# Kernel optimization log

Hardware: AMD Instinct MI355X
Metric: run time of the kernel (lower is better)

The kernel has to match this reference:

```python
import jax, jax.numpy as jnp
import numpy as np

N, C, K = 65536, 128, 16

def setup_inputs() -> dict:
    key = jax.random.key(0)
    ks = jax.random.split(key, 16)
    def w(k, i, o):
        return jax.random.normal(k, (i, o), dtype=jnp.float32) / np.sqrt(i)
    inp = {
        "x": jax.random.normal(ks[0], (N, C), dtype=jnp.float32),
        "coords": jax.random.normal(ks[1], (N, 3), dtype=jnp.float32) * 10.0,
        "neighbor_idx": jax.random.randint(ks[2], (N, K), 0, N, dtype=jnp.int32),
        # linear_top / linear_down (1x1 Minkowski convs, BN folded into affine)
        "W_top": w(ks[3], C, C), "b_top": jnp.zeros((C,), jnp.float32),
        "W_down": w(ks[4], C, C), "b_down": jnp.zeros((C,), jnp.float32),
        # phi (query), psi (key), alpha (value) 1x1 convs
        "W_phi": w(ks[5], C, C), "b_phi": jnp.zeros((C,), jnp.float32),
        "W_psi": w(ks[6], C, C), "b_psi": jnp.zeros((C,), jnp.float32),
        "W_alpha": w(ks[7], C, C), "b_alpha": jnp.zeros((C,), jnp.float32),
        # delta: positional-encoding MLP on relative xyz (3 -> C -> C)
        "W_d1": w(ks[8], 3, C), "b_d1": jnp.zeros((C,), jnp.float32),
        "W_d2": w(ks[9], C, C), "b_d2": jnp.zeros((C,), jnp.float32),
        # gamma: attention MLP (C -> C -> C), vector attention
        "W_g1": w(ks[10], C, C), "b_g1": jnp.zeros((C,), jnp.float32),
        "W_g2": w(ks[11], C, C), "b_g2": jnp.zeros((C,), jnp.float32),
    }
    return inp

def reference(x, coords, W_top, b_top, W_down, b_down, W_phi, b_phi, W_psi, b_psi,
              W_alpha, b_alpha, W_d1, b_d1, W_d2, b_d2, W_g1, b_g1, W_g2, b_g2,
              neighbor_idx):
    # linear_top
    h = x @ W_top + b_top                                  # (N, C)
    phi = h @ W_phi + b_phi                                # (N, C) query
    psi = h @ W_psi + b_psi                                # (N, C) key
    alpha = h @ W_alpha + b_alpha                          # (N, C) value
    # gather neighbor features / coords (irregular access)
    nb_psi = psi[neighbor_idx]                             # (N, K, C)
    nb_alpha = alpha[neighbor_idx]                         # (N, K, C)
    rel = coords[:, None, :] - coords[neighbor_idx]        # (N, K, 3)
    # delta: relative positional encoding MLP
    pos = jax.nn.relu(rel @ W_d1 + b_d1) @ W_d2 + b_d2     # (N, K, C)
    # vector attention: gamma(phi_i - psi_j + delta)
    attn_in = phi[:, None, :] - nb_psi + pos               # (N, K, C)
    logits = jax.nn.relu(attn_in @ W_g1 + b_g1) @ W_g2 + b_g2
    w = jax.nn.softmax(logits, axis=1)                     # softmax over K neighbors
    y = jnp.sum(w * (nb_alpha + pos), axis=1)              # (N, C)
    # linear_down + residual
    return y @ W_down + b_down + x
```

## Files before the change

kernel.cpp:

```cpp
#include <hip/hip_runtime.h>
#include <math.h>

#define C 128
#define K 16
#define M 4
#define ROWS 64

typedef unsigned short ushort_t;
typedef unsigned int u32;
typedef float f32x4 __attribute__((ext_vector_type(4)));
typedef _Float16 f16x8 __attribute__((ext_vector_type(8)));

union U8h { _Float16 h[8]; uint4 u; };

__device__ __forceinline__ float f16tof(ushort_t b) {
    _Float16 h = __builtin_bit_cast(_Float16, b); return (float)h;
}
__device__ __forceinline__ ushort_t ftof16(float f) {
    _Float16 h = (_Float16)f; return __builtin_bit_cast(ushort_t, h);
}
__device__ __forceinline__ f32x4 mfma16(f16x8 a, f16x8 b, f32x4 c) {
    return __builtin_amdgcn_mfma_f32_16x16x32_f16(a, b, c, 0, 0, 0);
}

__global__ __launch_bounds__(128) void k_prep(
    const float* __restrict__ s0, const float* __restrict__ s1,
    const float* __restrict__ s2, const float* __restrict__ s3,
    ushort_t* __restrict__ d0, ushort_t* __restrict__ d1,
    ushort_t* __restrict__ d2, ushort_t* __restrict__ d3)
{
    const int m = blockIdx.x >> 7, n = blockIdx.x & 127, e = threadIdx.x;
    const float* s = (m==0) ? s0 : (m==1) ? s1 : (m==2) ? s2 : s3;
    ushort_t*   d = (m==0) ? d0 : (m==1) ? d1 : (m==2) ? d2 : d3;
    d[n*C + e] = ftof16(s[e*C + n]);
}

__global__ __launch_bounds__(512) void k_qkv2(
    const float* __restrict__ x,
    const ushort_t* __restrict__ WTt, const float* __restrict__ bt,
    const ushort_t* __restrict__ WTp, const float* __restrict__ bp,
    const ushort_t* __restrict__ WTs, const float* __restrict__ bs,
    const ushort_t* __restrict__ WTa, const float* __restrict__ ba,
    ushort_t* __restrict__ phiB, ushort_t* __restrict__ psiB,
    ushort_t* __restrict__ alfB)
{
    __shared__ ushort_t sX[64*C];
    __shared__ ushort_t sH[64*C];
    const int tid = threadIdx.x, lane = tid & 63, wv = tid >> 6;
    const int ncol = (wv<<4) + (lane&15), arow = lane&15;
    const int kgrp = lane>>4, krow0 = kgrp<<3;
    const int r0 = blockIdx.x * 64;

    {
        const int rX = tid>>3, cX = (tid&7)<<4;
        const float* xp = &x[(size_t)(r0+rX)*C + cX];
        #pragma unroll
        for (int hf = 0; hf < 2; ++hf) {
            const float4 a  = *(const float4*)&xp[hf*8 + 0];
            const float4 b2 = *(const float4*)&xp[hf*8 + 4];
            U8h v;
            v.h[0]=(_Float16)a.x;  v.h[1]=(_Float16)a.y;
            v.h[2]=(_Float16)a.z;  v.h[3]=(_Float16)a.w;
            v.h[4]=(_Float16)b2.x; v.h[5]=(_Float16)b2.y;
            v.h[6]=(_Float16)b2.z; v.h[7]=(_Float16)b2.w;
            const int col = cX + hf*8;
            *(uint4*)&sX[(rX<<7) + (col ^ ((rX&7)<<3))] = v.u;
        }
    }
    __syncthreads();

    {
        f16x8 bf[4]; f32x4 hacc[4];
        #pragma unroll
        for (int kk = 0; kk < 4; ++kk)
            bf[kk] = *(const f16x8*)&WTt[(size_t)ncol*C + (kk<<5) + krow0];
        #pragma unroll
        for (int m = 0; m < 4; ++m) hacc[m] = (f32x4){0.f,0.f,0.f,0.f};
        __builtin_amdgcn_s_setprio(1);
        #pragma unroll
        for (int m = 0; m < 4; ++m)
            #pragma unroll
            for (int kk = 0; kk < 4; ++kk) {
                const int row = (m<<4) + arow;
                const f16x8 af = *(const f16x8*)&sX[(row<<7) + (((kk<<5)+krow0) ^ ((arow&7)<<3))];
                hacc[m] = mfma16(af, bf[kk], hacc[m]);
            }
        __builtin_amdgcn_s_setprio(0);
        const float btc = bt[ncol];
        #pragma unroll
        for (int m = 0; m < 4; ++m)
            #pragma unroll
            for (int r = 0; r < 4; ++r) {
                const int row = (m<<4) + (kgrp<<2) + r;
                sH[(row<<7) + (ncol ^ ((row&7)<<3))] = ftof16(hacc[m][r] + btc);
            }
    }
    __syncthreads();

#define OGEMM(WT_, b_, o_)                                                    \
    {                                                                         \
        f16x8 wf[4]; f32x4 oacc[4];                                           \
        _Pragma("unroll")                                                     \
        for (int kk = 0; kk < 4; ++kk)                                        \
            wf[kk] = *(const f16x8*)&WT_[(size_t)ncol*C + (kk<<5) + krow0];   \
        _Pragma("unroll")                                                     \
        for (int m = 0; m < 4; ++m) oacc[m] = (f32x4){0.f,0.f,0.f,0.f};      \
        __builtin_amdgcn_s_setprio(1);                                        \
        _Pragma("unroll")                                                     \
        for (int m = 0; m < 4; ++m)                                           \
            _Pragma("unroll")                                                 \
            for (int kk = 0; kk < 4; ++kk) {                                  \
                const int row = (m<<4) + arow;                                \
                const f16x8 af = *(const f16x8*)&sH[(row<<7) + (((kk<<5)+krow0) ^ ((arow&7)<<3))]; \
                oacc[m] = mfma16(af, wf[kk], oacc[m]);                        \
            }                                                                 \
        __builtin_amdgcn_s_setprio(0);                                        \
        const float bc = b_[ncol];                                            \
        _Pragma("unroll")                                                     \
        for (int m = 0; m < 4; ++m)                                           \
            _Pragma("unroll")                                                 \
            for (int r = 0; r < 4; ++r) {                                     \
                const int row = (m<<4) + (kgrp<<2) + r;                       \
                o_[(size_t)(r0+row)*C + ncol] = ftof16(oacc[m][r] + bc);      \
            }                                                                 \
    }
    OGEMM(WTp, bp, phiB)
    OGEMM(WTs, bs, psiB)
    OGEMM(WTa, ba, alfB)
#undef OGEMM
}

__global__ __launch_bounds__(512, 4) void k_attn7(
    const ushort_t* __restrict__ phiB, const ushort_t* __restrict__ psiB,
    const ushort_t* __restrict__ alfB,
    const float* __restrict__ coords, const int* __restrict__ nidx,
    const float* __restrict__ Wd1, const float* __restrict__ bd1,
    const ushort_t* __restrict__ WTd2, const float* __restrict__ bd2,
    const ushort_t* __restrict__ WTg1, const float* __restrict__ bg1,
    const ushort_t* __restrict__ WTg2,
    ushort_t* __restrict__ yB,
    int ngroups, int gpb)
{
    __shared__ ushort_t sT0[ROWS*C];
    __shared__ ushort_t sT1[ROWS*C];
    __shared__ ushort_t sA[ROWS*C];
    __shared__ float    sWd1[3][C];
    __shared__ float    sbd1v[C];

    const int tid  = threadIdx.x, lane = tid & 63, wv = tid >> 6;
    const int ncol = (wv<<4) + (lane&15);
    const int arow = lane & 15;
    const int kgrp = lane >> 4, krow0 = kgrp << 3;
    const int grow = tid >> 3;
    const int gpt  = grow >> 4;
    const int gk   = grow & 15;
    const int gc   = (tid & 7) << 4;

    const int g0 = blockIdx.x * gpb;
    if (g0 >= ngroups) return;
    const int gend = (g0 + gpb < ngroups) ? (g0 + gpb) : ngroups;

    if (tid < 3*C) ((float*)sWd1)[tid] = Wd1[tid];
    else if (tid < 4*C) sbd1v[tid - 3*C] = bd1[tid - 3*C];

    f16x8 wd2[4];
    #pragma unroll
    for (int kk = 0; kk < 4; ++kk)
        wd2[kk] = *(const f16x8*)&WTd2[(size_t)ncol*C + (kk<<5) + krow0];
    const float bd2c = bd2[ncol], bg1c = bg1[ncol];

    __syncthreads();

    int jP; float cn0,cn1,cn2,cj0,cj1,cj2;
    {
        const int pt = g0*M + gpt;
        jP  = nidx[(size_t)pt*K + gk];
        cn0 = coords[(size_t)pt*3+0]; cn1 = coords[(size_t)pt*3+1]; cn2 = coords[(size_t)pt*3+2];
        cj0 = coords[(size_t)jP*3+0]; cj1 = coords[(size_t)jP*3+1]; cj2 = coords[(size_t)jP*3+2];
    }

    const int si0 = (grow<<7) + (gc ^ ((grow&7)<<3));
    const int si1 = (grow<<7) + ((gc+8) ^ ((grow&7)<<3));

    for (int g = g0; g < gend; ++g) {
        const int p0 = g * M;
        const bool hn = (g + 1 < gend);

        {
            const float rx = cn0 - cj0, ry = cn1 - cj1, rz = cn2 - cj2;
            #pragma unroll
            for (int hf = 0; hf < 2; ++hf) {
                U8h hi, lo;
                #pragma unroll
                for (int z = 0; z < 8; ++z) {
                    const int c = gc + (hf<<3) + z;
                    float t = fmaf(rx, sWd1[0][c],
                              fmaf(ry, sWd1[1][c],
                              fmaf(rz, sWd1[2][c], sbd1v[c])));
                    t = fmaxf(t, 0.f);
                    hi.h[z] = (_Float16)t;
                    lo.h[z] = (_Float16)(t - (float)hi.h[z]);
                }
                const int si = hf ? si1 : si0;
                *(uint4*)&sT0[si] = hi.u;
                *(uint4*)&sT1[si] = lo.u;
            }
        }
        __syncthreads();

        ushort_t phv[M];
        ushort_t psv[M][4];
        #pragma unroll
        for (int m = 0; m < M; ++m) {
            phv[m] = phiB[(size_t)(p0+m)*C + ncol];
            const int4 j4 = *(const int4*)&nidx[(size_t)(p0+m)*K + (kgrp<<2)];
            psv[m][0] = psiB[(size_t)j4.x*C + ncol];
            psv[m][1] = psiB[(size_t)j4.y*C + ncol];
            psv[m][2] = psiB[(size_t)j4.z*C + ncol];
            psv[m][3] = psiB[(size_t)j4.w*C + ncol];
        }

        f32x4 pos[M];
        #pragma unroll
        for (int m = 0; m < M; ++m) pos[m] = (f32x4){0.f,0.f,0.f,0.f};
        __builtin_amdgcn_s_setprio(1);
        #pragma unroll
        for (int m = 0; m < M; ++m)
            #pragma unroll
            for (int kk = 0; kk < 4; ++kk) {
                const int si = (((m<<4)+arow)<<7) + (((kk<<5)+krow0) ^ ((arow&7)<<3));
                pos[m] = mfma16(*(const f16x8*)&sT0[si], wd2[kk], pos[m]);
                pos[m] = mfma16(*(const f16x8*)&sT1[si], wd2[kk], pos[m]);
            }
        __builtin_amdgcn_s_setprio(0);

        #pragma unroll
        for (int m = 0; m < M; ++m) {
            #pragma unroll
            for (int z = 0; z < 4; ++z) pos[m][z] += bd2c;
            const float phic = f16tof(phv[m]);
            #pragma unroll
            for (int r = 0; r < 4; ++r) {
                const int row = (m<<4) + (kgrp<<2) + r;
                const float av = phic - f16tof(psv[m][r]) + pos[m][r];
                sA[(row<<7) + (ncol ^ ((row&7)<<3))] = ftof16(av);
            }
        }
        __syncthreads();

        {
            f16x8 wg1s[4];
            #pragma unroll
            for (int kk = 0; kk < 4; ++kk)
                wg1s[kk] = *(const f16x8*)&WTg1[(size_t)ncol*C + (kk<<5) + krow0];

            f32x4 ua[M];
            #pragma unroll
            for (int m = 0; m < M; ++m) ua[m] = (f32x4){0.f,0.f,0.f,0.f};
            __builtin_amdgcn_s_setprio(1);
            #pragma unroll
            for (int m = 0; m < M; ++m)
                #pragma unroll
                for (int kk = 0; kk < 4; ++kk) {
                    const int si = (((m<<4)+arow)<<7) + (((kk<<5)+krow0) ^ ((arow&7)<<3));
                    ua[m] = mfma16(*(const f16x8*)&sA[si], wg1s[kk], ua[m]);
                }
            __builtin_amdgcn_s_setprio(0);
            #pragma unroll
            for (int m = 0; m < M; ++m)
                #pragma unroll
                for (int r = 0; r < 4; ++r) {
                    const int row = (m<<4) + (kgrp<<2) + r;
                    sT1[(row<<7) + (ncol ^ ((row&7)<<3))] =
                        ftof16(fmaxf(ua[m][r] + bg1c, 0.f));
                }
        }
        if (hn) {
            const int pt = (g+1)*M + gpt;
            jP  = nidx[(size_t)pt*K + gk];
            cn0 = coords[(size_t)pt*3+0]; cn1 = coords[(size_t)pt*3+1]; cn2 = coords[(size_t)pt*3+2];
            cj0 = coords[(size_t)jP*3+0]; cj1 = coords[(size_t)jP*3+1]; cj2 = coords[(size_t)jP*3+2];
        }
        __syncthreads();

        ushort_t alv[M][4];
        #pragma unroll
        for (int m = 0; m < M; ++m) {
            const int4 j4 = *(const int4*)&nidx[(size_t)(p0+m)*K + (kgrp<<2)];
            alv[m][0] = alfB[(size_t)j4.x*C + ncol];
            alv[m][1] = alfB[(size_t)j4.y*C + ncol];
            alv[m][2] = alfB[(size_t)j4.z*C + ncol];
            alv[m][3] = alfB[(size_t)j4.w*C + ncol];
        }
        f16x8 wg2s[4];
        #pragma unroll
        for (int kk = 0; kk < 4; ++kk)
            wg2s[kk] = *(const f16x8*)&WTg2[(size_t)ncol*C + (kk<<5) + krow0];

        f32x4 lg[M];
        #pragma unroll
        for (int m = 0; m < M; ++m) lg[m] = (f32x4){0.f,0.f,0.f,0.f};
        __builtin_amdgcn_s_setprio(1);
        #pragma unroll
        for (int m = 0; m < M; ++m)
            #pragma unroll
            for (int kk = 0; kk < 4; ++kk) {
                const int si = (((m<<4)+arow)<<7) + (((kk<<5)+krow0) ^ ((arow&7)<<3));
                lg[m] = mfma16(*(const f16x8*)&sT1[si], wg2s[kk], lg[m]);
            }
        __builtin_amdgcn_s_setprio(0);

        #pragma unroll
        for (int m = 0; m < M; ++m) {
            float mx = fmaxf(fmaxf(lg[m][0], lg[m][1]), fmaxf(lg[m][2], lg[m][3]));
            mx = fmaxf(mx, __shfl_xor(mx, 16));
            mx = fmaxf(mx, __shfl_xor(mx, 32));
            const float e0 = __expf(lg[m][0]-mx), e1 = __expf(lg[m][1]-mx);
            const float e2 = __expf(lg[m][2]-mx), e3 = __expf(lg[m][3]-mx);
            float den = e0 + e1 + e2 + e3;
            den += __shfl_xor(den, 16);
            den += __shfl_xor(den, 32);
            const float inv = 1.0f / den;
            float yp;
            yp  = e0 * (f16tof(alv[m][0]) + pos[m][0]);
            yp += e1 * (f16tof(alv[m][1]) + pos[m][1]);
            yp += e2 * (f16tof(alv[m][2]) + pos[m][2]);
            yp += e3 * (f16tof(alv[m][3]) + pos[m][3]);
            yp *= inv;
            yp += __shfl_xor(yp, 16);
            yp += __shfl_xor(yp, 32);
            if (lane < 16)
                yB[(size_t)(p0+m)*C + ncol] = ftof16(yp);
        }
        __syncthreads();
    }
}

__global__ __launch_bounds__(512) void k_down(
    const ushort_t* __restrict__ yB,
    const ushort_t* __restrict__ WTdn, const float* __restrict__ bdn,
    const float* __restrict__ x, float* __restrict__ out)
{
    __shared__ ushort_t sY[64*C];
    const int tid = threadIdx.x, lane = tid & 63, wv = tid >> 6;
    const int ncol = (wv<<4) + (lane&15), arow = lane&15;
    const int kgrp = lane>>4, krow0 = kgrp<<3;
    const int r0 = blockIdx.x * 64;

    {
        const int rY = tid>>3, cY = (tid&7)<<4;
        #pragma unroll
        for (int hf = 0; hf < 2; ++hf) {
            const uint4 v = *(const uint4*)&yB[(size_t)(r0+rY)*C + cY + hf*8];
            *(uint4*)&sY[(rY<<7) + ((cY + hf*8) ^ ((rY&7)<<3))] = v;
        }
    }
    __syncthreads();

    f16x8 wf[4]; f32x4 oacc[4];
    #pragma unroll
    for (int kk = 0; kk < 4; ++kk)
        wf[kk] = *(const f16x8*)&WTdn[(size_t)ncol*C + (kk<<5) + krow0];
    #pragma unroll
    for (int m = 0; m < 4; ++m) oacc[m] = (f32x4){0.f,0.f,0.f,0.f};
    __builtin_amdgcn_s_setprio(1);
    #pragma unroll
    for (int m = 0; m < 4; ++m)
        #pragma unroll
        for (int kk = 0; kk < 4; ++kk) {
            const int row = (m<<4) + arow;
            const f16x8 af = *(const f16x8*)&sY[(row<<7) + (((kk<<5)+krow0) ^ ((arow&7)<<3))];
            oacc[m] = mfma16(af, wf[kk], oacc[m]);
        }
    __builtin_amdgcn_s_setprio(0);
    const float bc = bdn[ncol];
    #pragma unroll
    for (int m = 0; m < 4; ++m)
        #pragma unroll
        for (int r = 0; r < 4; ++r) {
            const int row = (m<<4) + (kgrp<<2) + r;
            const size_t idx = (size_t)(r0+row)*C + ncol;
            out[idx] = oacc[m][r] + bc + x[idx];
        }
}

extern "C" void kernel_launch(void* const* d_in, const int* in_sizes, int n_in,
                              void* d_out, int out_size, void* d_ws, size_t ws_size,
                              hipStream_t stream)
{
    const float* x      = (const float*)d_in[0];
    const float* coords = (const float*)d_in[1];
    const int*   nidx   = (const int*)d_in[2];
    const float* W_top  = (const float*)d_in[3];
    const float* b_top  = (const float*)d_in[4];
    const float* W_down = (const float*)d_in[5];
    const float* b_down = (const float*)d_in[6];
    const float* W_phi  = (const float*)d_in[7];
    const float* b_phi  = (const float*)d_in[8];
    const float* W_psi  = (const float*)d_in[9];
    const float* b_psi  = (const float*)d_in[10];
    const float* W_alpha= (const float*)d_in[11];
    const float* b_alpha= (const float*)d_in[12];
    const float* W_d1   = (const float*)d_in[13];
    const float* b_d1   = (const float*)d_in[14];
    const float* W_d2   = (const float*)d_in[15];
    const float* b_d2   = (const float*)d_in[16];
    const float* W_g1   = (const float*)d_in[17];
    const float* b_g1   = (const float*)d_in[18];
    const float* W_g2   = (const float*)d_in[19];
    const float* b_g2   = (const float*)d_in[20];
    (void)b_g2;

    const int N = in_sizes[0] / C;

    ushort_t* WTt  = (ushort_t*)d_ws;
    ushort_t* WTp  = WTt  + C*C;
    ushort_t* WTs  = WTp  + C*C;
    ushort_t* WTa  = WTs  + C*C;
    ushort_t* WTd2 = WTa  + C*C;
    ushort_t* WTg1 = WTd2 + C*C;
    ushort_t* WTg2 = WTg1 + C*C;
    ushort_t* WTdn = WTg2 + C*C;
    ushort_t* phiB = WTdn + C*C;
    ushort_t* psiB = phiB + (size_t)N*C;
    ushort_t* alfB = psiB + (size_t)N*C;
    ushort_t* yB   = alfB + (size_t)N*C;
    float* out = (float*)d_out;

    hipLaunchKernelGGL(k_prep, dim3(4*C), dim3(C), 0, stream,
        W_top, W_phi, W_psi, W_alpha, WTt, WTp, WTs, WTa);
    hipLaunchKernelGGL(k_prep, dim3(4*C), dim3(C), 0, stream,
        W_d2, W_g1, W_g2, W_down, WTd2, WTg1, WTg2, WTdn);

    hipLaunchKernelGGL(k_qkv2, dim3(N / 64), dim3(512), 0, stream,
        x, WTt, b_top, WTp, b_phi, WTs, b_psi, WTa, b_alpha,
        phiB, psiB, alfB);

    const int ngroups = N / M;
    const int NBLK = 2048;
    const int gpb = (ngroups + NBLK - 1) / NBLK;
    hipLaunchKernelGGL(k_attn7, dim3(NBLK), dim3(512), 0, stream,
        phiB, psiB, alfB, coords, nidx,
        W_d1, b_d1, WTd2, b_d2, WTg1, b_g1, WTg2,
        yB, ngroups, gpb);

    hipLaunchKernelGGL(k_down, dim3(N / 64), dim3(512), 0, stream,
        yB, WTdn, b_down, x, out);
}
```

Before: 544.2 us.

## Restructure attention kernel to 256 threads, 2 points per group, two column tiles per wave

The attention kernel now runs 256-thread blocks handling 2 points (32 rows) per iteration, and each wave covers two 16-column tiles. A-operand fragments are loaded from LDS once and reused across both tiles, while weight fragments are reloaded from global memory per tile. The hi/lo fp16 split of the positional hidden layer is dropped, halving the delta-MLP MFMAs at some precision cost. Positional encodings are stashed in a new LDS buffer instead of registers, and the grid doubles to 4096 blocks. The intent is better occupancy and less register pressure, at the cost of extra global weight loads and an extra LDS round-trip.

```diff
diff --git a/kernel.cpp b/kernel.cpp
--- a/kernel.cpp
+++ b/kernel.cpp
@@ -3,8 +3,8 @@
 
 #define C 128
 #define K 16
-#define M 4
-#define ROWS 64
+#define M 2
+#define ROWS 32
 
 typedef unsigned short ushort_t;
 typedef unsigned int u32;
@@ -130,7 +130,7 @@
 #undef OGEMM
 }
 
-__global__ __launch_bounds__(512, 4) void k_attn7(
+__global__ __launch_bounds__(256, 3) void k_attn9(
     const ushort_t* __restrict__ phiB, const ushort_t* __restrict__ psiB,
     const ushort_t* __restrict__ alfB,
     const float* __restrict__ coords, const int* __restrict__ nidx,
@@ -141,14 +141,13 @@
     ushort_t* __restrict__ yB,
     int ngroups, int gpb)
 {
-    __shared__ ushort_t sT0[ROWS*C];
-    __shared__ ushort_t sT1[ROWS*C];
+    __shared__ ushort_t sT[ROWS*C];
     __shared__ ushort_t sA[ROWS*C];
-    __shared__ float    sWd1[3][C];
-    __shared__ float    sbd1v[C];
+    __shared__ ushort_t sP[ROWS*C];
+    __shared__ float    sW1b[512];
 
     const int tid  = threadIdx.x, lane = tid & 63, wv = tid >> 6;
-    const int ncol = (wv<<4) + (lane&15);
+    const int col0 = (wv<<4) + (lane&15);
     const int arow = lane & 15;
     const int kgrp = lane >> 4, krow0 = kgrp << 3;
     const int grow = tid >> 3;
@@ -160,14 +159,12 @@
     if (g0 >= ngroups) return;
     const int gend = (g0 + gpb < ngroups) ? (g0 + gpb) : ngroups;
 
-    if (tid < 3*C) ((float*)sWd1)[tid] = Wd1[tid];
-    else if (tid < 4*C) sbd1v[tid - 3*C] = bd1[tid - 3*C];
-
-    f16x8 wd2[4];
-    #pragma unroll
-    for (int kk = 0; kk < 4; ++kk)
-        wd2[kk] = *(const f16x8*)&WTd2[(size_t)ncol*C + (kk<<5) + krow0];
-    const float bd2c = bd2[ncol], bg1c = bg1[ncol];
+    for (int i = tid; i < 512; i += 256)
+        sW1b[i] = (i < 384) ? Wd1[i] : bd1[i - 384];
+
+    float bd2c[2], bg1c[2];
+    bd2c[0] = bd2[col0]; bd2c[1] = bd2[col0+64];
+    bg1c[0] = bg1[col0]; bg1c[1] = bg1[col0+64];
 
     __syncthreads();
 
@@ -179,9 +176,6 @@
         cj0 = coords[(size_t)jP*3+0]; cj1 = coords[(size_t)jP*3+1]; cj2 = coords[(size_t)jP*3+2];
     }
 
-    const int si0 = (grow<<7) + (gc ^ ((grow&7)<<3));
-    const int si1 = (grow<<7) + ((gc+8) ^ ((grow&7)<<3));
-
     for (int g = g0; g < gend; ++g) {
         const int p0 = g * M;
         const bool hn = (g + 1 < gend);
@@ -189,91 +183,106 @@
         {
             const float rx = cn0 - cj0, ry = cn1 - cj1, rz = cn2 - cj2;
             #pragma unroll
-            for (int hf = 0; hf < 2; ++hf) {
-                U8h hi, lo;
+            for (int s = 0; s < 2; ++s) {
+                U8h h;
                 #pragma unroll
                 for (int z = 0; z < 8; ++z) {
-                    const int c = gc + (hf<<3) + z;
-                    float t = fmaf(rx, sWd1[0][c],
-                              fmaf(ry, sWd1[1][c],
-                              fmaf(rz, sWd1[2][c], sbd1v[c])));
-                    t = fmaxf(t, 0.f);
-                    hi.h[z] = (_Float16)t;
-                    lo.h[z] = (_Float16)(t - (float)hi.h[z]);
+                    const int c = gc + (s<<3) + z;
+                    float t = fmaf(rx, sW1b[c],
+                              fmaf(ry, sW1b[128+c],
+                              fmaf(rz, sW1b[256+c], sW1b[384+c])));
+                    h.h[z] = (_Float16)fmaxf(t, 0.f);
                 }
-                const int si = hf ? si1 : si0;
-                *(uint4*)&sT0[si] = hi.u;
-                *(uint4*)&sT1[si] = lo.u;
+                *(uint4*)&sT[(grow<<7) + ((gc + (s<<3)) ^ ((grow&7)<<3))] = h.u;
             }
         }
         __syncthreads();
 
-        ushort_t phv[M];
-        ushort_t psv[M][4];
-        #pragma unroll
-        for (int m = 0; m < M; ++m) {
-            phv[m] = phiB[(size_t)(p0+m)*C + ncol];
-            const int4 j4 = *(const int4*)&nidx[(size_t)(p0+m)*K + (kgrp<<2)];
-            psv[m][0] = psiB[(size_t)j4.x*C + ncol];
-            psv[m][1] = psiB[(size_t)j4.y*C + ncol];
-            psv[m][2] = psiB[(size_t)j4.z*C + ncol];
-            psv[m][3] = psiB[(size_t)j4.w*C + ncol];
-        }
-
-        f32x4 pos[M];
-        #pragma unroll
-        for (int m = 0; m < M; ++m) pos[m] = (f32x4){0.f,0.f,0.f,0.f};
-        __builtin_amdgcn_s_setprio(1);
-        #pragma unroll
-        for (int m = 0; m < M; ++m)
-            #pragma unroll
-            for (int kk = 0; kk < 4; ++kk) {
-                const int si = (((m<<4)+arow)<<7) + (((kk<<5)+krow0) ^ ((arow&7)<<3));
-                pos[m] = mfma16(*(const f16x8*)&sT0[si], wd2[kk], pos[m]);
-                pos[m] = mfma16(*(const f16x8*)&sT1[si], wd2[kk], pos[m]);
-            }
-        __builtin_amdgcn_s_setprio(0);
-
-        #pragma unroll
-        for (int m = 0; m < M; ++m) {
-            #pragma unroll
-            for (int z = 0; z < 4; ++z) pos[m][z] += bd2c;
-            const float phic = f16tof(phv[m]);
-            #pragma unroll
-            for (int r = 0; r < 4; ++r) {
-                const int row = (m<<4) + (kgrp<<2) + r;
-                const float av = phic - f16tof(psv[m][r]) + pos[m][r];
-                sA[(row<<7) + (ncol ^ ((row&7)<<3))] = ftof16(av);
+        {
+            f16x8 af[M][4];
+            #pragma unroll
+            for (int m = 0; m < M; ++m)
+                #pragma unroll
+                for (int kk = 0; kk < 4; ++kk)
+                    af[m][kk] = *(const f16x8*)&sT[(((m<<4)+arow)<<7) + (((kk<<5)+krow0) ^ ((arow&7)<<3))];
+
+            #pragma unroll
+            for (int ct = 0; ct < 2; ++ct) {
+                const int col = col0 + (ct<<6);
+                f16x8 wf[4];
+                #pragma unroll
+                for (int kk = 0; kk < 4; ++kk)
+                    wf[kk] = *(const f16x8*)&WTd2[(size_t)col*C + (kk<<5) + krow0];
+                ushort_t phv[M], psv[M][4];
+                #pragma unroll
+                for (int m = 0; m < M; ++m) {
+                    phv[m] = phiB[(size_t)(p0+m)*C + col];
+                    const int4 j4 = *(const int4*)&nidx[(size_t)(p0+m)*K + (kgrp<<2)];
+                    psv[m][0] = psiB[(size_t)j4.x*C + col];
+                    psv[m][1] = psiB[(size_t)j4.y*C + col];
+                    psv[m][2] = psiB[(size_t)j4.z*C + col];
+                    psv[m][3] = psiB[(size_t)j4.w*C + col];
+                }
+                f32x4 pos[M];
+                #pragma unroll
+                for (int m = 0; m < M; ++m) pos[m] = (f32x4){0.f,0.f,0.f,0.f};
+                __builtin_amdgcn_s_setprio(1);
+                #pragma unroll
+                for (int m = 0; m < M; ++m)
+                    #pragma unroll
+                    for (int kk = 0; kk < 4; ++kk)
+                        pos[m] = mfma16(af[m][kk], wf[kk], pos[m]);
+                __builtin_amdgcn_s_setprio(0);
+                #pragma unroll
+                for (int m = 0; m < M; ++m) {
+                    const float ph = f16tof(phv[m]);
+                    #pragma unroll
+                    for (int r = 0; r < 4; ++r) {
+                        const int row = (m<<4) + (kgrp<<2) + r;
+                        const int si  = (row<<7) + (col ^ ((row&7)<<3));
+                        const float pv = pos[m][r] + bd2c[ct];
+                        sP[si] = ftof16(pv);
+                        sA[si] = ftof16(ph - f16tof(psv[m][r]) + pv);
+                    }
+                }
             }
         }
         __syncthreads();
 
         {
-            f16x8 wg1s[4];
-            #pragma unroll
-            for (int kk = 0; kk < 4; ++kk)
-                wg1s[kk] = *(const f16x8*)&WTg1[(size_t)ncol*C + (kk<<5) + krow0];
-
-            f32x4 ua[M];
-            #pragma unroll
-            for (int m = 0; m < M; ++m) ua[m] = (f32x4){0.f,0.f,0.f,0.f};
-            __builtin_amdgcn_s_setprio(1);
+            f16x8 af[M][4];
             #pragma unroll
             for (int m = 0; m < M; ++m)
                 #pragma unroll
-                for (int kk = 0; kk < 4; ++kk) {
-                    const int si = (((m<<4)+arow)<<7) + (((kk<<5)+krow0) ^ ((arow&7)<<3));
-                    ua[m] = mfma16(*(const f16x8*)&sA[si], wg1s[kk], ua[m]);
-                }
-            __builtin_amdgcn_s_setprio(0);
-            #pragma unroll
-            for (int m = 0; m < M; ++m)
-                #pragma unroll
-                for (int r = 0; r < 4; ++r) {
-                    const int row = (m<<4) + (kgrp<<2) + r;
-                    sT1[(row<<7) + (ncol ^ ((row&7)<<3))] =
-                        ftof16(fmaxf(ua[m][r] + bg1c, 0.f));
-                }
+                for (int kk = 0; kk < 4; ++kk)
+                    af[m][kk] = *(const f16x8*)&sA[(((m<<4)+arow)<<7) + (((kk<<5)+krow0) ^ ((arow&7)<<3))];
+
+            #pragma unroll
+            for (int ct = 0; ct < 2; ++ct) {
+                const int col = col0 + (ct<<6);
+                f16x8 wf[4];
+                #pragma unroll
+                for (int kk = 0; kk < 4; ++kk)
+                    wf[kk] = *(const f16x8*)&WTg1[(size_t)col*C + (kk<<5) + krow0];
+                f32x4 ua[M];
+                #pragma unroll
+                for (int m = 0; m < M; ++m) ua[m] = (f32x4){0.f,0.f,0.f,0.f};
+                __builtin_amdgcn_s_setprio(1);
+                #pragma unroll
+                for (int m = 0; m < M; ++m)
+                    #pragma unroll
+                    for (int kk = 0; kk < 4; ++kk)
+                        ua[m] = mfma16(af[m][kk], wf[kk], ua[m]);
+                __builtin_amdgcn_s_setprio(0);
+                #pragma unroll
+                for (int m = 0; m < M; ++m)
+                    #pragma unroll
+                    for (int r = 0; r < 4; ++r) {
+                        const int row = (m<<4) + (kgrp<<2) + r;
+                        sT[(row<<7) + (col ^ ((row&7)<<3))] =
+                            ftof16(fmaxf(ua[m][r] + bg1c[ct], 0.f));
+                    }
+            }
         }
         if (hn) {
             const int pt = (g+1)*M + gpt;
@@ -283,54 +292,70 @@
         }
         __syncthreads();
 
-        ushort_t alv[M][4];
-        #pragma unroll
-        for (int m = 0; m < M; ++m) {
-            const int4 j4 = *(const int4*)&nidx[(size_t)(p0+m)*K + (kgrp<<2)];
-            alv[m][0] = alfB[(size_t)j4.x*C + ncol];
-            alv[m][1] = alfB[(size_t)j4.y*C + ncol];
-            alv[m][2] = alfB[(size_t)j4.z*C + ncol];
-            alv[m][3] = alfB[(size_t)j4.w*C + ncol];
-        }
-        f16x8 wg2s[4];
-        #pragma unroll
-        for (int kk = 0; kk < 4; ++kk)
-            wg2s[kk] = *(const f16x8*)&WTg2[(size_t)ncol*C + (kk<<5) + krow0];
-
-        f32x4 lg[M];
-        #pragma unroll
-        for (int m = 0; m < M; ++m) lg[m] = (f32x4){0.f,0.f,0.f,0.f};
-        __builtin_amdgcn_s_setprio(1);
-        #pragma unroll
-        for (int m = 0; m < M; ++m)
-            #pragma unroll
-            for (int kk = 0; kk < 4; ++kk) {
-                const int si = (((m<<4)+arow)<<7) + (((kk<<5)+krow0) ^ ((arow&7)<<3));
-                lg[m] = mfma16(*(const f16x8*)&sT1[si], wg2s[kk], lg[m]);
-            }
-        __builtin_amdgcn_s_setprio(0);
-
-        #pragma unroll
-        for (int m = 0; m < M; ++m) {
-            float mx = fmaxf(fmaxf(lg[m][0], lg[m][1]), fmaxf(lg[m][2], lg[m][3]));
-            mx = fmaxf(mx, __shfl_xor(mx, 16));
-            mx = fmaxf(mx, __shfl_xor(mx, 32));
-            const float e0 = __expf(lg[m][0]-mx), e1 = __expf(lg[m][1]-mx);
-            const float e2 = __expf(lg[m][2]-mx), e3 = __expf(lg[m][3]-mx);
-            float den = e0 + e1 + e2 + e3;
-            den += __shfl_xor(den, 16);
-            den += __shfl_xor(den, 32);
-            const float inv = 1.0f / den;
-            float yp;
-            yp  = e0 * (f16tof(alv[m][0]) + pos[m][0]);
-            yp += e1 * (f16tof(alv[m][1]) + pos[m][1]);
-            yp += e2 * (f16tof(alv[m][2]) + pos[m][2]);
-            yp += e3 * (f16tof(alv[m][3]) + pos[m][3]);
-            yp *= inv;
-            yp += __shfl_xor(yp, 16);
-            yp += __shfl_xor(yp, 32);
-            if (lane < 16)
-                yB[(size_t)(p0+m)*C + ncol] = ftof16(yp);
+        {
+            f16x8 af[M][4];
+            #pragma unroll
+            for (int m = 0; m < M; ++m)
+                #pragma unroll
+                for (int kk = 0; kk < 4; ++kk)
+                    af[m][kk] = *(const f16x8*)&sT[(((m<<4)+arow)<<7) + (((kk<<5)+krow0) ^ ((arow&7)<<3))];
+
+            #pragma unroll
+            for (int ct = 0; ct < 2; ++ct) {
+                const int col = col0 + (ct<<6);
+                f16x8 wf[4];
+                #pragma unroll
+                for (int kk = 0; kk < 4; ++kk)
+                    wf[kk] = *(const f16x8*)&WTg2[(size_t)col*C + (kk<<5) + krow0];
+                ushort_t alv[M][4];
+                #pragma unroll
+                for (int m = 0; m < M; ++m) {
+                    const int4 j4 = *(const int4*)&nidx[(size_t)(p0+m)*K + (kgrp<<2)];
+                    alv[m][0] = alfB[(size_t)j4.x*C + col];
+                    alv[m][1] = alfB[(size_t)j4.y*C + col];
+                    alv[m][2] = alfB[(size_t)j4.z*C + col];
+                    alv[m][3] = alfB[(size_t)j4.w*C + col];
+                }
+                f32x4 lg[M];
+                #pragma unroll
+                for (int m = 0; m < M; ++m) lg[m] = (f32x4){0.f,0.f,0.f,0.f};
+                __builtin_amdgcn_s_setprio(1);
+                #pragma unroll
+                for (int m = 0; m < M; ++m)
+                    #pragma unroll
+                    for (int kk = 0; kk < 4; ++kk)
+                        lg[m] = mfma16(af[m][kk], wf[kk], lg[m]);
+                __builtin_amdgcn_s_setprio(0);
+
+                #pragma unroll
+                for (int m = 0; m < M; ++m) {
+                    float mx = fmaxf(fmaxf(lg[m][0], lg[m][1]), fmaxf(lg[m][2], lg[m][3]));
+                    mx = fmaxf(mx, __shfl_xor(mx, 16));
+                    mx = fmaxf(mx, __shfl_xor(mx, 32));
+                    const float e0 = __expf(lg[m][0]-mx), e1 = __expf(lg[m][1]-mx);
+                    const float e2 = __expf(lg[m][2]-mx), e3 = __expf(lg[m][3]-mx);
+                    float den = e0 + e1 + e2 + e3;
+                    den += __shfl_xor(den, 16);
+                    den += __shfl_xor(den, 32);
+                    const float inv = 1.0f / den;
+                    float pr[4];
+                    #pragma unroll
+                    for (int r = 0; r < 4; ++r) {
+                        const int row = (m<<4) + (kgrp<<2) + r;
+                        pr[r] = f16tof(sP[(row<<7) + (col ^ ((row&7)<<3))]);
+                    }
+                    float yp;
+                    yp  = e0 * (f16tof(alv[m][0]) + pr[0]);
+                    yp += e1 * (f16tof(alv[m][1]) + pr[1]);
+                    yp += e2 * (f16tof(alv[m][2]) + pr[2]);
+                    yp += e3 * (f16tof(alv[m][3]) + pr[3]);
+                    yp *= inv;
+                    yp += __shfl_xor(yp, 16);
+                    yp += __shfl_xor(yp, 32);
+                    if (lane < 16)
+                        yB[(size_t)(p0+m)*C + col] = ftof16(yp);
+                }
+            }
         }
         __syncthreads();
     }
@@ -437,9 +462,9 @@
         phiB, psiB, alfB);
 
     const int ngroups = N / M;
-    const int NBLK = 2048;
+    const int NBLK = 4096;
     const int gpb = (ngroups + NBLK - 1) / NBLK;
-    hipLaunchKernelGGL(k_attn7, dim3(NBLK), dim3(512), 0, stream,
+    hipLaunchKernelGGL(k_attn9, dim3(NBLK), dim3(256), 0, stream,
         phiB, psiB, alfB, coords, nidx,
         W_d1, b_d1, WTd2, b_d2, WTg1, b_g1, WTg2,
         yB, ngroups, gpb);
```

Measured after the change: 1.065 ms. +95.6%, slower.
